# Performance work log

Hardware: AMD Instinct MI355X
Metric: run time of the kernel (lower is better)

Reference implementation:

```python
import jax, jax.numpy as jnp
import numpy as np

B, S, D, H, L, FF, V, TYPES = 16, 512, 1024, 16, 8, 4096, 30522, 2
DH = D // H
BETA = 1.0          # pbit_temperature
EPS = 1e-12         # layer_norm_eps
STD = 0.02          # initializer_range


def _ln(x, g, b):
    m = x.mean(-1, keepdims=True)
    v = ((x - m) ** 2).mean(-1, keepdims=True)
    return (x - m) * jax.lax.rsqrt(v + EPS) * g + b


def setup_inputs() -> dict:
    key = jax.random.key(0)
    ks = iter(jax.random.split(key, 32))
    rn = lambda shape: (jax.random.normal(next(ks), shape, dtype=jnp.float32) * STD)
    inp = {
        'input_ids': jax.random.randint(next(ks), (B, S), 0, V),
        'token_type_ids': jax.random.randint(next(ks), (B, S), 0, TYPES),
        'tok_emb': rn((V, D)),
        'pos_emb': rn((S, D)),
        'type_emb': rn((TYPES, D)),
        'emb_g': jnp.ones((D,), jnp.float32),
        'emb_b': jnp.zeros((D,), jnp.float32),
        # stacked per-layer parameters [L, ...]
        'Wq': rn((L, D, D)), 'bq': jnp.zeros((L, D), jnp.float32),
        'Wk': rn((L, D, D)), 'bk': jnp.zeros((L, D), jnp.float32),
        'Wv': rn((L, D, D)), 'bv': jnp.zeros((L, D), jnp.float32),
        'Wo': rn((L, D, D)), 'bo': jnp.zeros((L, D), jnp.float32),
        'ln1_g': jnp.ones((L, D), jnp.float32), 'ln1_b': jnp.zeros((L, D), jnp.float32),
        'ln2_g': jnp.ones((L, D), jnp.float32), 'ln2_b': jnp.zeros((L, D), jnp.float32),
        'W1': rn((L, D, FF)), 'b1': jnp.zeros((L, FF), jnp.float32),
        'W2': rn((L, FF, D)), 'b2': jnp.zeros((L, D), jnp.float32),
    }
    return inp


def reference(input_ids, token_type_ids, tok_emb, pos_emb, type_emb, emb_g, emb_b,
              Wq, bq, Wk, bk, Wv, bv, Wo, bo, ln1_g, ln1_b, ln2_g, ln2_b,
              W1, b1, W2, b2):
    # Embeddings (eval mode: TSU noise + dropout are identity)
    h = tok_emb[input_ids] + pos_emb[None, :, :] + type_emb[token_type_ids]
    h = _ln(h, emb_g, emb_b)

    def layer(h, p):
        wq, bq_, wk, bk_, wv, bv_, wo, bo_, g1, bb1, g2, bb2, w1, bf1, w2, bf2 = p
        x = _ln(h, g1, bb1)  # pre-LN per TinyBioBERTLayer
        q = (x @ wq + bq_).reshape(B, S, H, DH)
        k = (x @ wk + bk_).reshape(B, S, H, DH)
        v = (x @ wv + bv_).reshape(B, S, H, DH)
        # P-bit attention in expectation == temperature-scaled softmax SDPA
        scores = jnp.einsum('bqhd,bkhd->bhqk', q, k) * (BETA / np.sqrt(DH))
        a = jax.nn.softmax(scores, axis=-1)
        ctx = jnp.einsum('bhqk,bkhd->bqhd', a, v).reshape(B, S, D)
        h = h + ctx @ wo + bo_
        y = _ln(h, g2, bb2)
        y = jax.nn.gelu(y @ w1 + bf1, approximate=False) @ w2 + bf2
        return h + y, None

    params = (Wq, bq, Wk, bk, Wv, bv, Wo, bo, ln1_g, ln1_b, ln2_g, ln2_b, W1, b1, W2, b2)
    h, _ = jax.lax.scan(layer, h, params)
    return h
```

## Files before the change

kernel.cpp:

```cpp
#include <hip/hip_runtime.h>
#include <math.h>

#define B_  16
#define S_  512
#define D_  1024
#define H_  16
#define DH_ 64
#define L_  8
#define FF_ 4096
#define M_  (B_*S_)

typedef __attribute__((ext_vector_type(4))) float  f32x4;
typedef __attribute__((ext_vector_type(8))) short  s8v;
typedef __attribute__((ext_vector_type(4))) short  s4v;
typedef __attribute__((ext_vector_type(8))) __bf16 bf8v;

__device__ __forceinline__ short f2bf(float f) {
  union { float f; unsigned u; } x; x.f = f;
  unsigned r = x.u + 0x7fffu + ((x.u >> 16) & 1u);
  return (short)(r >> 16);
}

__device__ __forceinline__ f32x4 mfma16(s8v a, s8v b, f32x4 c) {
  return __builtin_amdgcn_mfma_f32_16x16x32_bf16(
      __builtin_bit_cast(bf8v, a), __builtin_bit_cast(bf8v, b), c, 0, 0, 0);
}

__device__ __forceinline__ void gl_lds16(const void* g, void* lds) {
  __builtin_amdgcn_global_load_lds(
      (const __attribute__((address_space(1))) unsigned int*)g,
      (__attribute__((address_space(3))) unsigned int*)lds, 16, 0, 0);
}

__device__ __forceinline__ float gelu_f(float v) {
  const float t  = 0.7978845608f * (v + 0.044715f * v * v * v);
  const float e  = __expf(-2.0f * fabsf(t));
  const float th = copysignf((1.f - e) / (1.f + e), t);
  return 0.5f * v * (1.0f + th);
}

__global__ __launch_bounds__(256) void tcvt(const float* __restrict__ src,
                                            short* __restrict__ dst, int R, int C,
                                            size_t dls) {
  __shared__ float tile[32][33];
  src += (size_t)blockIdx.z * R * C;
  dst += (size_t)blockIdx.z * dls;
  const int c0 = blockIdx.x * 32, r0 = blockIdx.y * 32;
  const int tx = threadIdx.x & 31, ty = threadIdx.x >> 5;
#pragma unroll
  for (int i = 0; i < 32; i += 8)
    tile[ty + i][tx] = src[(size_t)(r0 + ty + i) * C + (c0 + tx)];
  __syncthreads();
#pragma unroll
  for (int i = 0; i < 32; i += 8)
    dst[(size_t)(c0 + ty + i) * R + (r0 + tx)] = f2bf(tile[tx][ty + i]);
}

__global__ __launch_bounds__(256) void embed_ln(
    const int* __restrict__ ids, const int* __restrict__ tts,
    const float* __restrict__ tok, const float* __restrict__ pos,
    const float* __restrict__ typ, const float* __restrict__ g,
    const float* __restrict__ bta, float* __restrict__ h) {
  const int row = blockIdx.x;
  const int s = row & (S_ - 1);
  const int id = ids[row], tt = tts[row];
  const int t = threadIdx.x;
  const float4 a = ((const float4*)(tok + (size_t)id * D_))[t];
  const float4 p = ((const float4*)(pos + (size_t)s  * D_))[t];
  const float4 y = ((const float4*)(typ + (size_t)tt * D_))[t];
  float x0 = a.x + p.x + y.x, x1 = a.y + p.y + y.y;
  float x2 = a.z + p.z + y.z, x3 = a.w + p.w + y.w;
  float sum = x0 + x1 + x2 + x3;
  float sq  = x0*x0 + x1*x1 + x2*x2 + x3*x3;
  __shared__ float red[8];
#pragma unroll
  for (int d = 1; d < 64; d <<= 1) { sum += __shfl_xor(sum, d); sq += __shfl_xor(sq, d); }
  if ((t & 63) == 0) { red[t >> 6] = sum; red[(t >> 6) + 4] = sq; }
  __syncthreads();
  sum = red[0] + red[1] + red[2] + red[3];
  sq  = red[4] + red[5] + red[6] + red[7];
  const float mean = sum * (1.f / D_);
  const float var  = sq * (1.f / D_) - mean * mean;
  const float rstd = rsqrtf(fmaxf(var, 0.f) + 1e-12f);
  const float4 gg = ((const float4*)g)[t];
  const float4 bb = ((const float4*)bta)[t];
  float4 o;
  o.x = (x0 - mean) * rstd * gg.x + bb.x;
  o.y = (x1 - mean) * rstd * gg.y + bb.y;
  o.z = (x2 - mean) * rstd * gg.z + bb.z;
  o.w = (x3 - mean) * rstd * gg.w + bb.w;
  ((float4*)(h + (size_t)row * D_))[t] = o;
}

__global__ __launch_bounds__(256) void ln_bf16(
    const float* __restrict__ h, const float* __restrict__ g,
    const float* __restrict__ bta, short* __restrict__ out) {
  const int row = blockIdx.x;
  const int t = threadIdx.x;
  const float4 x = ((const float4*)(h + (size_t)row * D_))[t];
  float sum = x.x + x.y + x.z + x.w;
  float sq  = x.x*x.x + x.y*x.y + x.z*x.z + x.w*x.w;
  __shared__ float red[8];
#pragma unroll
  for (int d = 1; d < 64; d <<= 1) { sum += __shfl_xor(sum, d); sq += __shfl_xor(sq, d); }
  if ((t & 63) == 0) { red[t >> 6] = sum; red[(t >> 6) + 4] = sq; }
  __syncthreads();
  sum = red[0] + red[1] + red[2] + red[3];
  sq  = red[4] + red[5] + red[6] + red[7];
  const float mean = sum * (1.f / D_);
  const float var  = sq * (1.f / D_) - mean * mean;
  const float rstd = rsqrtf(fmaxf(var, 0.f) + 1e-12f);
  const float4 gg = ((const float4*)g)[t];
  const float4 bb = ((const float4*)bta)[t];
  s4v o;
  o[0] = f2bf((x.x - mean) * rstd * gg.x + bb.x);
  o[1] = f2bf((x.y - mean) * rstd * gg.y + bb.y);
  o[2] = f2bf((x.z - mean) * rstd * gg.z + bb.z);
  o[3] = f2bf((x.w - mean) * rstd * gg.w + bb.w);
  *(s4v*)&out[(size_t)row * D_ + t * 4] = o;
}

template<int MODE>
__global__ __launch_bounds__(512, 1) void gemm8(
    const short* __restrict__ A, const short* __restrict__ Bt,
    const float* __restrict__ b0, const float* __restrict__ b1,
    const float* __restrict__ b2, short* __restrict__ out,
    float* __restrict__ hres, int N, int K, int LD, int nby) {
  __shared__ __align__(16) char lds[131072];
  const int tid = threadIdx.x, wid = tid >> 6, lane = tid & 63;
  const int wr = wid >> 2, wc = wid & 3;
  const int l15 = lane & 15, l4 = lane >> 4;

  const int n8 = (int)gridDim.x >> 3;
  const int bid = (int)blockIdx.x;
  const int xcd = bid & 7, tt_ = bid >> 3;
  const int cpx = n8 / nby;
  const int bx = xcd * cpx + tt_ / nby;
  const int by = tt_ % nby;

  const short* __restrict__ Ab = A + (size_t)bx * 256 * LD;
  const short* __restrict__ Bb = Bt + (size_t)by * 256 * LD;

  const int str0 = tid >> 3;
  const int stc  = (((tid & 7) ^ (str0 & 7)) * 8);
  const int r7  = l15 & 7;
  const int kx0 = ((l4) ^ r7) * 16;
  const int kx1 = ((4 + l4) ^ r7) * 16;
  const int arow = (wr * 128 + l15) * 128;
  const int brow = (wc * 64 + l15) * 128;

  f32x4 acc[8][4];
#pragma unroll
  for (int m = 0; m < 8; ++m)
#pragma unroll
    for (int n = 0; n < 4; ++n) acc[m][n] = f32x4{0.f, 0.f, 0.f, 0.f};
  s8v af[8][2], bf[4][2];

  const int nt = K >> 6, it = nt >> 1;

#define BAR_ __builtin_amdgcn_s_barrier()
#define LGKM0_ asm volatile("s_waitcnt lgkmcnt(0)" ::: "memory")
#define VMC_(n) asm volatile("s_waitcnt vmcnt(" #n ")" ::: "memory")
#define ST_(isB, slot, hh, kt) do { \
    const short* _g = ((isB) ? Bb : Ab) + (size_t)((hh) * 128 + str0) * LD + ((kt) << 6) + stc; \
    char* _d = lds + ((isB) ? 65536 : 0) + (slot) * 32768 + (hh) * 16384 + wid * 1024; \
    gl_lds16(_g, _d); \
    gl_lds16(_g + (size_t)64 * LD, _d + 8192); \
  } while (0)
#define RDA4_(slot, g) do { \
    const char* _p = lds + (slot) * 32768 + arow + (g) * 8192; \
    _Pragma("unroll") for (int _i = 0; _i < 4; ++_i) { \
      af[(g)*4+_i][0] = *(const s8v*)(_p + _i * 2048 + kx0); \
      af[(g)*4+_i][1] = *(const s8v*)(_p + _i * 2048 + kx1); } \
  } while (0)
#define RDB2_(slot, g) do { \
    const char* _p = lds + 65536 + (slot) * 32768 + brow + (g) * 4096; \
    _Pragma("unroll") for (int _i = 0; _i < 2; ++_i) { \
      bf[(g)*2+_i][0] = *(const s8v*)(_p + _i * 2048 + kx0); \
      bf[(g)*2+_i][1] = *(const s8v*)(_p + _i * 2048 + kx1); } \
  } while (0)
#define MM_(mq, nq) do { \
    __builtin_amdgcn_s_setprio(1); \
    _Pragma("unroll") for (int _mf = 0; _mf < 4; ++_mf) \
    _Pragma("unroll") for (int _nf = 0; _nf < 2; ++_nf) \
    _Pragma("unroll") for (int _ks = 0; _ks < 2; ++_ks) \
      acc[(mq)*4+_mf][(nq)*2+_nf] = \
        mfma16(bf[(nq)*2+_nf][_ks], af[(mq)*4+_mf][_ks], acc[(mq)*4+_mf][(nq)*2+_nf]); \
    __builtin_amdgcn_s_setprio(0); \
  } while (0)

  ST_(1,0,0,0); ST_(1,0,1,0); ST_(0,0,0,0); ST_(0,0,1,0);
  ST_(1,1,0,1); ST_(0,1,0,1); ST_(0,1,1,1);
  VMC_(6);
  BAR_;

  for (int t = 0; t < it; ++t) {
    const int ka = 2 * t, kb = ka + 1;
    const bool s2 = (ka + 2) < nt, s3 = (kb + 2) < nt;
    RDA4_(0, 0); RDB2_(0, 0);
    ST_(1, 1, 1, kb);
    BAR_; LGKM0_; MM_(0, 0); BAR_;
    RDB2_(0, 1);
    BAR_; LGKM0_; MM_(0, 1); BAR_;
    RDA4_(0, 1);
    if (s2) ST_(1, 0, 0, ka + 2);
    BAR_; LGKM0_; MM_(1, 0); BAR_;
    if (s2) { ST_(1, 0, 1, ka + 2); VMC_(4); } else { VMC_(0); }
    BAR_; MM_(1, 1); BAR_;
    RDA4_(1, 0); RDB2_(1, 0);
    if (s2) ST_(0, 0, 0, ka + 2);
    BAR_; LGKM0_; MM_(0, 0); BAR_;
    RDB2_(1, 1);
    if (s2) ST_(0, 0, 1, ka + 2);
    BAR_; LGKM0_; MM_(0, 1); BAR_;
    RDA4_(1, 1);
    if (s3) ST_(1, 1, 0, kb + 2);
    BAR_; LGKM0_; MM_(1, 0); BAR_;
    if (s3) { ST_(0, 1, 0, kb + 2); ST_(0, 1, 1, kb + 2); VMC_(6); }
    BAR_; MM_(1, 1); BAR_;
  }

  const int r0 = bx * 256 + wr * 128;
  const int c0 = by * 256 + wc * 64;
  const int which = (MODE == 3) ? (c0 >> 10) : 0;
  const float* __restrict__ bias =
      (MODE == 3) ? (which == 0 ? b0 : (which == 1 ? b1 : b2)) : b0;
  short* __restrict__ outw = (MODE == 3) ? out + (size_t)which * M_ * D_ : out;
#pragma unroll
  for (int n = 0; n < 4; ++n) {
    const int colb = c0 + n * 16 + l4 * 4;
    const int colw = colb & (D_ - 1);
    float4 bb4 = {0.f, 0.f, 0.f, 0.f};
    if (MODE == 3)       bb4 = *(const float4*)&bias[colw];
    else if (bias)       bb4 = *(const float4*)&bias[colb];
#pragma unroll
    for (int m = 0; m < 8; ++m) {
      const int row = r0 + m * 16 + l15;
      float v0 = acc[m][n][0] + bb4.x, v1 = acc[m][n][1] + bb4.y;
      float v2 = acc[m][n][2] + bb4.z, v3 = acc[m][n][3] + bb4.w;
      if (MODE == 2) {
        float4* hp = (float4*)&hres[(size_t)row * N + colb];
        float4 hv = *hp;
        hv.x += v0; hv.y += v1; hv.z += v2; hv.w += v3;
        *hp = hv;
      } else {
        if (MODE == 1) { v0 = gelu_f(v0); v1 = gelu_f(v1); v2 = gelu_f(v2); v3 = gelu_f(v3); }
        s4v pk;
        pk[0] = f2bf(v0); pk[1] = f2bf(v1); pk[2] = f2bf(v2); pk[3] = f2bf(v3);
        if (MODE == 3) {
          const int b = row >> 9, s = row & 511, hd = colw >> 6, dh = colw & 63;
          *(s4v*)&outw[((((size_t)b * H_ + hd) * S_ + s) << 6) + dh] = pk;
        } else {
          *(s4v*)&outw[(size_t)row * N + colb] = pk;
        }
      }
    }
  }
#undef BAR_
#undef LGKM0_
#undef VMC_
#undef ST_
#undef RDA4_
#undef RDB2_
#undef MM_
}

__global__ __launch_bounds__(256, 2) void attn(
    const short* __restrict__ Q, const short* __restrict__ K,
    const short* __restrict__ V, short* __restrict__ ctx) {
  __shared__ __align__(16) short Kl[32][72];
  __shared__ __align__(16) short Vt[DH_][40];
  __shared__ __align__(16) short Pl[4][32 * 40];

  const int tid = threadIdx.x, wid = tid >> 6, lane = tid & 63;
  const int l15 = lane & 15, l4 = lane >> 4;
  const int bh = blockIdx.y;
  const size_t base = (size_t)bh * S_ * DH_;
  const short* Qb = Q + base;
  const short* Kb = K + base;
  const short* Vb = V + base;

  const int qoff = blockIdx.x * 128 + wid * 32;

  s8v qf[2][2];
#pragma unroll
  for (int mf = 0; mf < 2; ++mf)
#pragma unroll
    for (int ks = 0; ks < 2; ++ks)
      qf[mf][ks] = *(const s8v*)&Qb[(size_t)(qoff + mf * 16 + l15) * DH_ + ks * 32 + l4 * 8];

  const f32x4 zero4 = {0.f, 0.f, 0.f, 0.f};
  f32x4 o[2][4];
  float rm[2][4], rs[2][4];
#pragma unroll
  for (int mf = 0; mf < 2; ++mf) {
#pragma unroll
    for (int nf = 0; nf < 4; ++nf) o[mf][nf] = zero4;
#pragma unroll
    for (int r = 0; r < 4; ++r) { rm[mf][r] = -1e30f; rs[mf][r] = 0.f; }
  }

  const int str = tid >> 3;
  const int stc = (tid & 7) * 8;

  for (int kt = 0; kt < S_ / 32; ++kt) {
    __syncthreads();
    {
      const s8v kk = *(const s8v*)&Kb[(size_t)(kt * 32 + str) * DH_ + stc];
      *(s8v*)&Kl[str][stc] = kk;
      const s8v vv = *(const s8v*)&Vb[(size_t)(kt * 32 + str) * DH_ + stc];
#pragma unroll
      for (int j = 0; j < 8; ++j) Vt[stc + j][str] = vv[j];
    }
    __syncthreads();

    f32x4 sc[2][2];
#pragma unroll
    for (int mf = 0; mf < 2; ++mf)
#pragma unroll
      for (int nt = 0; nt < 2; ++nt) sc[mf][nt] = zero4;
#pragma unroll
    for (int nt = 0; nt < 2; ++nt)
#pragma unroll
      for (int ks = 0; ks < 2; ++ks) {
        const s8v kf = *(const s8v*)&Kl[nt * 16 + l15][ks * 32 + l4 * 8];
#pragma unroll
        for (int mf = 0; mf < 2; ++mf)
          sc[mf][nt] = mfma16(qf[mf][ks], kf, sc[mf][nt]);
      }

#pragma unroll
    for (int mf = 0; mf < 2; ++mf) {
      float tm[4];
#pragma unroll
      for (int r = 0; r < 4; ++r) {
        sc[mf][0][r] *= 0.125f; sc[mf][1][r] *= 0.125f;
        tm[r] = fmaxf(sc[mf][0][r], sc[mf][1][r]);
      }
#pragma unroll
      for (int d = 1; d < 16; d <<= 1)
#pragma unroll
        for (int r = 0; r < 4; ++r) tm[r] = fmaxf(tm[r], __shfl_xor(tm[r], d));
      float ps[4];
#pragma unroll
      for (int r = 0; r < 4; ++r) {
        const float nm = fmaxf(rm[mf][r], tm[r]);
        const float so = __expf(rm[mf][r] - nm);
        rm[mf][r] = nm;
        rs[mf][r] *= so;
#pragma unroll
        for (int nf = 0; nf < 4; ++nf) o[mf][nf][r] *= so;
        const float p0 = __expf(sc[mf][0][r] - nm);
        const float p1 = __expf(sc[mf][1][r] - nm);
        sc[mf][0][r] = p0; sc[mf][1][r] = p1;
        ps[r] = p0 + p1;
      }
#pragma unroll
      for (int d = 1; d < 16; d <<= 1)
#pragma unroll
        for (int r = 0; r < 4; ++r) ps[r] += __shfl_xor(ps[r], d);
#pragma unroll
      for (int r = 0; r < 4; ++r) rs[mf][r] += ps[r];
#pragma unroll
      for (int nt = 0; nt < 2; ++nt)
#pragma unroll
        for (int r = 0; r < 4; ++r)
          Pl[wid][(mf * 16 + l4 * 4 + r) * 40 + nt * 16 + l15] = f2bf(sc[mf][nt][r]);
    }
    asm volatile("s_waitcnt lgkmcnt(0)" ::: "memory");

    s8v vf[4];
#pragma unroll
    for (int nf = 0; nf < 4; ++nf)
      vf[nf] = *(const s8v*)&Vt[nf * 16 + l15][l4 * 8];
#pragma unroll
    for (int mf = 0; mf < 2; ++mf) {
      const s8v pf = *(const s8v*)&Pl[wid][(mf * 16 + l15) * 40 + l4 * 8];
#pragma unroll
      for (int nf = 0; nf < 4; ++nf)
        o[mf][nf] = mfma16(pf, vf[nf], o[mf][nf]);
    }
  }

  const int bb = bh >> 4, hh = bh & 15;
#pragma unroll
  for (int mf = 0; mf < 2; ++mf)
#pragma unroll
    for (int r = 0; r < 4; ++r) {
      const int qrow = qoff + mf * 16 + l4 * 4 + r;
      const float inv = 1.0f / rs[mf][r];
      short* dst = ctx + (size_t)(bb * S_ + qrow) * D_ + hh * DH_;
#pragma unroll
      for (int nf = 0; nf < 4; ++nf)
        dst[nf * 16 + l15] = f2bf(o[mf][nf][r] * inv);
    }
}

extern "C" void kernel_launch(void* const* d_in, const int* in_sizes, int n_in,
                              void* d_out, int out_size, void* d_ws, size_t ws_size,
                              hipStream_t stream) {
  const int*   ids = (const int*)d_in[0];
  const int*   tts = (const int*)d_in[1];
  const float* tok = (const float*)d_in[2];
  const float* pos = (const float*)d_in[3];
  const float* typ = (const float*)d_in[4];
  const float* eg  = (const float*)d_in[5];
  const float* eb  = (const float*)d_in[6];
  const float* Wq  = (const float*)d_in[7];  const float* bq = (const float*)d_in[8];
  const float* Wk  = (const float*)d_in[9];  const float* bk = (const float*)d_in[10];
  const float* Wv  = (const float*)d_in[11]; const float* bv = (const float*)d_in[12];
  const float* Wo  = (const float*)d_in[13]; const float* bo = (const float*)d_in[14];
  const float* g1  = (const float*)d_in[15]; const float* be1 = (const float*)d_in[16];
  const float* g2  = (const float*)d_in[17]; const float* be2 = (const float*)d_in[18];
  const float* W1  = (const float*)d_in[19]; const float* b1 = (const float*)d_in[20];
  const float* W2  = (const float*)d_in[21]; const float* b2 = (const float*)d_in[22];

  float* h = (float*)d_out;

  const size_t szDD  = (size_t)D_ * D_;
  const size_t szDF  = (size_t)D_ * FF_;
  const size_t xb_b  = (size_t)M_ * D_ * 2;
  const size_t big_b = (size_t)M_ * FF_ * 2;
  const size_t wfull = (szDD * 4 + szDF * 2) * 2 * L_;
  const bool full = ws_size >= wfull + xb_b + big_b + 8192;

  char* p = (char*)d_ws;
  auto alloc = [&](size_t bytes) { char* r = p; p += (bytes + 255) & ~(size_t)255; return r; };
  const size_t wl = full ? L_ : 1;
  short* wqkvT = (short*)alloc(szDD * 3 * 2 * wl);
  short* woT   = (short*)alloc(szDD * 2 * wl);
  short* w1T   = (short*)alloc(szDF * 2 * wl);
  short* w2T   = (short*)alloc(szDF * 2 * wl);
  short* xb  = (short*)alloc(xb_b);
  char*  big = alloc(big_b);
  short* qb  = (short*)big;
  short* cb  = xb;
  short* tb  = (short*)big;

  if (full) {
    tcvt<<<dim3(D_/32,  D_/32,  L_), 256, 0, stream>>>(Wq, wqkvT,          D_,  D_,  3*szDD);
    tcvt<<<dim3(D_/32,  D_/32,  L_), 256, 0, stream>>>(Wk, wqkvT +   szDD, D_,  D_,  3*szDD);
    tcvt<<<dim3(D_/32,  D_/32,  L_), 256, 0, stream>>>(Wv, wqkvT + 2*szDD, D_,  D_,  3*szDD);
    tcvt<<<dim3(D_/32,  D_/32,  L_), 256, 0, stream>>>(Wo, woT, D_,  D_,  szDD);
    tcvt<<<dim3(FF_/32, D_/32,  L_), 256, 0, stream>>>(W1, w1T, D_,  FF_, szDF);
    tcvt<<<dim3(D_/32,  FF_/32, L_), 256, 0, stream>>>(W2, w2T, FF_, D_,  szDF);
  }

  embed_ln<<<M_, 256, 0, stream>>>(ids, tts, tok, pos, typ, eg, eb, h);

  const int nbx = M_ / 256;
  for (int l = 0; l < L_; ++l) {
    if (!full) {
      tcvt<<<dim3(D_/32,  D_/32,  1), 256, 0, stream>>>(Wq + (size_t)l*szDD, wqkvT,          D_,  D_,  0);
      tcvt<<<dim3(D_/32,  D_/32,  1), 256, 0, stream>>>(Wk + (size_t)l*szDD, wqkvT +   szDD, D_,  D_,  0);
      tcvt<<<dim3(D_/32,  D_/32,  1), 256, 0, stream>>>(Wv + (size_t)l*szDD, wqkvT + 2*szDD, D_,  D_,  0);
      tcvt<<<dim3(D_/32,  D_/32,  1), 256, 0, stream>>>(Wo + (size_t)l*szDD, woT, D_,  D_,  0);
      tcvt<<<dim3(FF_/32, D_/32,  1), 256, 0, stream>>>(W1 + (size_t)l*szDF, w1T, D_,  FF_, 0);
      tcvt<<<dim3(D_/32,  FF_/32, 1), 256, 0, stream>>>(W2 + (size_t)l*szDF, w2T, FF_, D_,  0);
    }
    const size_t o3 = full ? (size_t)l * 3 * szDD : 0;
    const size_t od = full ? (size_t)l * szDD : 0;
    const size_t of = full ? (size_t)l * szDF : 0;

    ln_bf16<<<M_, 256, 0, stream>>>(h, g1 + l*D_, be1 + l*D_, xb);
    gemm8<3><<<nbx * (3*D_/256), 512, 0, stream>>>(
        xb, wqkvT + o3, bq + l*D_, bk + l*D_, bv + l*D_, qb, nullptr, 3*D_, D_, D_, 3*D_/256);
    attn<<<dim3(S_/128, B_*H_), 256, 0, stream>>>(
        qb, qb + (size_t)M_*D_, qb + 2*(size_t)M_*D_, cb);
    gemm8<2><<<nbx * (D_/256), 512, 0, stream>>>(
        cb, woT + od, bo + l*D_, nullptr, nullptr, nullptr, h, D_, D_, D_, D_/256);
    ln_bf16<<<M_, 256, 0, stream>>>(h, g2 + l*D_, be2 + l*D_, xb);
    gemm8<1><<<nbx * (FF_/256), 512, 0, stream>>>(
        xb, w1T + of, b1 + l*FF_, nullptr, nullptr, tb, nullptr, FF_, D_, D_, FF_/256);
    gemm8<2><<<nbx * (D_/256), 512, 0, stream>>>(
        tb, w2T + of, b2 + l*D_, nullptr, nullptr, nullptr, h, D_, FF_, FF_, D_/256);
  }
}
```

Baseline: 3.513 ms.

## Split-K the Wo and W2 GEMMs into two partials reduced inside the LayerNorm

```diff
diff --git a/kernel.cpp b/kernel.cpp
--- a/kernel.cpp
+++ b/kernel.cpp
@@ -120,6 +120,58 @@
   *(s4v*)&out[(size_t)row * D_ + t * 4] = o;
 }
 
+__global__ __launch_bounds__(256) void ln_red(
+    float* __restrict__ h, const float* __restrict__ p0,
+    const float* __restrict__ p1, const float* __restrict__ badd,
+    const float* __restrict__ g, const float* __restrict__ bta,
+    short* __restrict__ out) {
+  const int row = blockIdx.x;
+  const int t = threadIdx.x;
+  const size_t off = (size_t)row * D_;
+  float4 x = ((const float4*)(h + off))[t];
+  const float4 a = ((const float4*)(p0 + off))[t];
+  const float4 b = ((const float4*)(p1 + off))[t];
+  const float4 c = ((const float4*)badd)[t];
+  x.x += a.x + b.x + c.x; x.y += a.y + b.y + c.y;
+  x.z += a.z + b.z + c.z; x.w += a.w + b.w + c.w;
+  ((float4*)(h + off))[t] = x;
+  float sum = x.x + x.y + x.z + x.w;
+  float sq  = x.x*x.x + x.y*x.y + x.z*x.z + x.w*x.w;
+  __shared__ float red[8];
+#pragma unroll
+  for (int d = 1; d < 64; d <<= 1) { sum += __shfl_xor(sum, d); sq += __shfl_xor(sq, d); }
+  if ((t & 63) == 0) { red[t >> 6] = sum; red[(t >> 6) + 4] = sq; }
+  __syncthreads();
+  sum = red[0] + red[1] + red[2] + red[3];
+  sq  = red[4] + red[5] + red[6] + red[7];
+  const float mean = sum * (1.f / D_);
+  const float var  = sq * (1.f / D_) - mean * mean;
+  const float rstd = rsqrtf(fmaxf(var, 0.f) + 1e-12f);
+  const float4 gg = ((const float4*)g)[t];
+  const float4 bb = ((const float4*)bta)[t];
+  s4v o;
+  o[0] = f2bf((x.x - mean) * rstd * gg.x + bb.x);
+  o[1] = f2bf((x.y - mean) * rstd * gg.y + bb.y);
+  o[2] = f2bf((x.z - mean) * rstd * gg.z + bb.z);
+  o[3] = f2bf((x.w - mean) * rstd * gg.w + bb.w);
+  *(s4v*)&out[off + t * 4] = o;
+}
+
+__global__ __launch_bounds__(256) void final_add(
+    float* __restrict__ h, const float* __restrict__ p0,
+    const float* __restrict__ p1, const float* __restrict__ badd) {
+  const int row = blockIdx.x;
+  const int t = threadIdx.x;
+  const size_t off = (size_t)row * D_;
+  float4 x = ((const float4*)(h + off))[t];
+  const float4 a = ((const float4*)(p0 + off))[t];
+  const float4 b = ((const float4*)(p1 + off))[t];
+  const float4 c = ((const float4*)badd)[t];
+  x.x += a.x + b.x + c.x; x.y += a.y + b.y + c.y;
+  x.z += a.z + b.z + c.z; x.w += a.w + b.w + c.w;
+  ((float4*)(h + off))[t] = x;
+}
+
 template<int MODE>
 __global__ __launch_bounds__(512, 1) void gemm8(
     const short* __restrict__ A, const short* __restrict__ Bt,
@@ -134,12 +186,15 @@
   const int n8 = (int)gridDim.x >> 3;
   const int bid = (int)blockIdx.x;
   const int xcd = bid & 7, tt_ = bid >> 3;
-  const int cpx = n8 / nby;
-  const int bx = xcd * cpx + tt_ / nby;
-  const int by = tt_ % nby;
-
-  const short* __restrict__ Ab = A + (size_t)bx * 256 * LD;
-  const short* __restrict__ Bb = Bt + (size_t)by * 256 * LD;
+  const int nbv = (MODE == 4) ? nby * 2 : nby;
+  const int cpx = n8 / nbv;
+  const int bx = xcd * cpx + tt_ / nbv;
+  const int bv = tt_ % nbv;
+  const int by = (MODE == 4) ? (bv & 3) : bv;
+  const int slice = (MODE == 4) ? (bv >> 2) : 0;
+
+  const short* __restrict__ Ab = A + (size_t)bx * 256 * LD + (size_t)slice * K;
+  const short* __restrict__ Bb = Bt + (size_t)by * 256 * LD + (size_t)slice * K;
 
   const int str0 = tid >> 3;
   const int stc  = (((tid & 7) ^ (str0 & 7)) * 8);
@@ -226,13 +281,15 @@
   const float* __restrict__ bias =
       (MODE == 3) ? (which == 0 ? b0 : (which == 1 ? b1 : b2)) : b0;
   short* __restrict__ outw = (MODE == 3) ? out + (size_t)which * M_ * D_ : out;
+  float* __restrict__ pp =
+      (MODE == 4) ? hres + (size_t)slice * ((size_t)M_ * D_) : hres;
 #pragma unroll
   for (int n = 0; n < 4; ++n) {
     const int colb = c0 + n * 16 + l4 * 4;
     const int colw = colb & (D_ - 1);
     float4 bb4 = {0.f, 0.f, 0.f, 0.f};
-    if (MODE == 3)       bb4 = *(const float4*)&bias[colw];
-    else if (bias)       bb4 = *(const float4*)&bias[colb];
+    if (MODE == 3)                       bb4 = *(const float4*)&bias[colw];
+    else if (MODE != 4 && bias)          bb4 = *(const float4*)&bias[colb];
 #pragma unroll
     for (int m = 0; m < 8; ++m) {
       const int row = r0 + m * 16 + l15;
@@ -243,6 +300,9 @@
         float4 hv = *hp;
         hv.x += v0; hv.y += v1; hv.z += v2; hv.w += v3;
         *hp = hv;
+      } else if (MODE == 4) {
+        float4 pv; pv.x = v0; pv.y = v1; pv.z = v2; pv.w = v3;
+        *(float4*)&pp[(size_t)row * N + colb] = pv;
       } else {
         if (MODE == 1) { v0 = gelu_f(v0); v1 = gelu_f(v1); v2 = gelu_f(v2); v3 = gelu_f(v3); }
         s4v pk;
@@ -421,8 +481,10 @@
   const size_t szDF  = (size_t)D_ * FF_;
   const size_t xb_b  = (size_t)M_ * D_ * 2;
   const size_t big_b = (size_t)M_ * FF_ * 2;
+  const size_t pa_b  = (size_t)M_ * D_ * 4;
   const size_t wfull = (szDD * 4 + szDF * 2) * 2 * L_;
   const bool full = ws_size >= wfull + xb_b + big_b + 8192;
+  const bool sk   = ws_size >= wfull + xb_b + big_b + 2 * pa_b + 8192;
 
   char* p = (char*)d_ws;
   auto alloc = [&](size_t bytes) { char* r = p; p += (bytes + 255) & ~(size_t)255; return r; };
@@ -433,6 +495,8 @@
   short* w2T   = (short*)alloc(szDF * 2 * wl);
   short* xb  = (short*)alloc(xb_b);
   char*  big = alloc(big_b);
+  float* pa0 = sk ? (float*)alloc(pa_b) : nullptr;
+  float* pa1 = sk ? (float*)alloc(pa_b) : nullptr;
   short* qb  = (short*)big;
   short* cb  = xb;
   short* tb  = (short*)big;
@@ -462,17 +526,39 @@
     const size_t od = full ? (size_t)l * szDD : 0;
     const size_t of = full ? (size_t)l * szDF : 0;
 
-    ln_bf16<<<M_, 256, 0, stream>>>(h, g1 + l*D_, be1 + l*D_, xb);
+    if (l == 0 || !sk)
+      ln_bf16<<<M_, 256, 0, stream>>>(h, g1 + l*D_, be1 + l*D_, xb);
+    else
+      ln_red<<<M_, 256, 0, stream>>>(h, pa0, pa1, b2 + (l-1)*D_,
+                                     g1 + l*D_, be1 + l*D_, xb);
+
     gemm8<3><<<nbx * (3*D_/256), 512, 0, stream>>>(
         xb, wqkvT + o3, bq + l*D_, bk + l*D_, bv + l*D_, qb, nullptr, 3*D_, D_, D_, 3*D_/256);
     attn<<<dim3(S_/128, B_*H_), 256, 0, stream>>>(
         qb, qb + (size_t)M_*D_, qb + 2*(size_t)M_*D_, cb);
-    gemm8<2><<<nbx * (D_/256), 512, 0, stream>>>(
-        cb, woT + od, bo + l*D_, nullptr, nullptr, nullptr, h, D_, D_, D_, D_/256);
-    ln_bf16<<<M_, 256, 0, stream>>>(h, g2 + l*D_, be2 + l*D_, xb);
+
+    if (sk) {
+      gemm8<4><<<nbx * (D_/256) * 2, 512, 0, stream>>>(
+          cb, woT + od, nullptr, nullptr, nullptr, nullptr, pa0, D_, D_/2, D_, D_/256);
+      ln_red<<<M_, 256, 0, stream>>>(h, pa0, pa1, bo + l*D_,
+                                     g2 + l*D_, be2 + l*D_, xb);
+    } else {
+      gemm8<2><<<nbx * (D_/256), 512, 0, stream>>>(
+          cb, woT + od, bo + l*D_, nullptr, nullptr, nullptr, h, D_, D_, D_, D_/256);
+      ln_bf16<<<M_, 256, 0, stream>>>(h, g2 + l*D_, be2 + l*D_, xb);
+    }
+
     gemm8<1><<<nbx * (FF_/256), 512, 0, stream>>>(
         xb, w1T + of, b1 + l*FF_, nullptr, nullptr, tb, nullptr, FF_, D_, D_, FF_/256);
-    gemm8<2><<<nbx * (D_/256), 512, 0, stream>>>(
-        tb, w2T + of, b2 + l*D_, nullptr, nullptr, nullptr, h, D_, FF_, FF_, D_/256);
+
+    if (sk) {
+      gemm8<4><<<nbx * (D_/256) * 2, 512, 0, stream>>>(
+          tb, w2T + of, nullptr, nullptr, nullptr, nullptr, pa0, D_, FF_/2, FF_, D_/256);
+    } else {
+      gemm8<2><<<nbx * (D_/256), 512, 0, stream>>>(
+          tb, w2T + of, b2 + l*D_, nullptr, nullptr, nullptr, h, D_, FF_, FF_, D_/256);
+    }
   }
-}
+  if (sk)
+    final_add<<<M_, 256, 0, stream>>>(h, pa0, pa1, b2 + (L_-1)*D_);
+}
```

Result: faster. 3.188 ms (-9.3%).
